# Kernel optimization log

Hardware: AMD Instinct MI355X
Metric: run time of the kernel (lower is better)

The kernel has to match this reference:

```python
import jax, jax.numpy as jnp
import numpy as np

N, E, G = 50000, 1600000, 512
IN_DIM, HEADS, C1, C2, HIDDEN = 128, 3, 32, 32, 512
NEG_SLOPE = 0.2
EPS = 1e-16


def _glorot(key, shape):
    fan_in = shape[0]
    return jax.random.normal(key, shape, dtype=jnp.float32) / np.sqrt(fan_in)


def setup_inputs() -> dict:
    key = jax.random.key(0)
    ks = jax.random.split(key, 16)
    x = jax.random.normal(ks[0], (N, IN_DIM), dtype=jnp.float32)
    edge_index = jax.random.randint(ks[1], (2, E), 0, N, dtype=jnp.int64)
    batch = (jnp.arange(N, dtype=jnp.int64) * G) // N  # sorted, all graphs non-empty
    d1, d2 = HEADS * C1, HEADS * C2
    return {
        "x": x,
        "W_l1": _glorot(ks[2], (IN_DIM, d1)), "b_l1": jnp.zeros((d1,), jnp.float32),
        "W_r1": _glorot(ks[3], (IN_DIM, d1)), "b_r1": jnp.zeros((d1,), jnp.float32),
        "att1": _glorot(ks[4], (HEADS, C1)), "bias1": jnp.zeros((d1,), jnp.float32),
        "W_l2": _glorot(ks[5], (d1, d2)), "b_l2": jnp.zeros((d2,), jnp.float32),
        "W_r2": _glorot(ks[6], (d1, d2)), "b_r2": jnp.zeros((d2,), jnp.float32),
        "att2": _glorot(ks[7], (HEADS, C2)), "bias2": jnp.zeros((d2,), jnp.float32),
        "W_fc1": _glorot(ks[8], (d1 + d2, HIDDEN)), "b_fc1": jnp.zeros((HIDDEN,), jnp.float32),
        "W_fc2": _glorot(ks[9], (HIDDEN, 2)), "b_fc2": jnp.zeros((2,), jnp.float32),
        "edge_index": edge_index,
        "batch": batch,
    }


def gatv2_conv(xin, src, dst, W_l, b_l, W_r, b_r, att, bias, heads, out_c):
    n = xin.shape[0]
    x_l = (xin @ W_l + b_l).reshape(n, heads, out_c)  # source-side projection
    x_r = (xin @ W_r + b_r).reshape(n, heads, out_c)  # target-side projection
    e = jax.nn.leaky_relu(x_l[src] + x_r[dst], NEG_SLOPE)  # [E', H, C]
    logits = jnp.einsum("ehc,hc->eh", e, att)  # [E', H]
    m = jax.ops.segment_max(logits, dst, num_segments=n)
    a = jnp.exp(logits - m[dst])
    denom = jax.ops.segment_sum(a, dst, num_segments=n)
    alpha = a / (denom[dst] + EPS)  # per-destination edge softmax (PyG semantics)
    out = jax.ops.segment_sum(x_l[src] * alpha[:, :, None], dst, num_segments=n)
    return out.reshape(n, heads * out_c) + bias


def reference(x, W_l1, b_l1, W_r1, b_r1, att1, bias1,
              W_l2, b_l2, W_r2, b_r2, att2, bias2,
              W_fc1, b_fc1, W_fc2, b_fc2, edge_index, batch):
    n = x.shape[0]
    loop = jnp.arange(n, dtype=edge_index.dtype)
    src = jnp.concatenate([edge_index[0], loop])  # PyG GATv2Conv adds self-loops
    dst = jnp.concatenate([edge_index[1], loop])
    h1 = jnp.tanh(gatv2_conv(x, src, dst, W_l1, b_l1, W_r1, b_r1, att1, bias1, HEADS, C1))
    h2 = jnp.tanh(gatv2_conv(h1, src, dst, W_l2, b_l2, W_r2, b_r2, att2, bias2, HEADS, C2))
    h = jnp.concatenate([h1, h2], axis=1)  # [N, (C1+C2)*H]
    first_idx = jnp.searchsorted(batch, jnp.arange(G, dtype=batch.dtype))  # first node of each graph
    pooled = h[first_idx]  # [G, (C1+C2)*H]
    hidden = jax.nn.relu(pooled @ W_fc1 + b_fc1)
    logits = hidden @ W_fc2 + b_fc2
    return jax.nn.log_softmax(logits, axis=1)
```

## Files before the change

kernel.cpp:

```cpp
#include <hip/hip_runtime.h>
#include <hip/hip_bf16.h>
#include <hip/hip_fp16.h>
#include <math.h>

#define NN 50000
#define EE 1600000
#define GG 512
#define INDIM 128
#define HEADS 3
#define CC 32
#define DD 96
#define HID 512
#define NEG 0.2f
#define EPS_DEN 1e-16f
#define CAP 128

#define OFF_WL1   0
#define OFF_BL1   12288
#define OFF_WR1   12384
#define OFF_BR1   24672
#define OFF_ATT1  24768
#define OFF_BIAS1 24864
#define OFF_WL2   24960
#define OFF_BL2   34176
#define OFF_WR2   34272
#define OFF_BR2   43488
#define OFF_ATT2  43584
#define OFF_BIAS2 43680
#define OFF_WFC1  43776
#define OFF_BFC1  142080
#define OFF_WFC2  142592
#define OFF_BFC2  143616
#define P_TOTAL   143744

typedef _Float16 h8 __attribute__((ext_vector_type(8)));
typedef float f4 __attribute__((ext_vector_type(4)));

static __device__ __forceinline__ float bf2f(__hip_bfloat16 v) { return __bfloat162float(v); }

static __device__ __forceinline__ int getI(const void* p, long long i, bool w64) {
    return w64 ? ((const int*)p)[2 * i] : ((const int*)p)[i];
}

__global__ void detect_kernel(const void* __restrict__ x, const void* __restrict__ ei,
                              int* __restrict__ flags)
{
    __shared__ int wild, zcnt;
    if (threadIdx.x == 0) { wild = 0; zcnt = 0; }
    __syncthreads();
    int w = 0, z = 0;
    const __hip_bfloat16* xb = (const __hip_bfloat16*)x;
    for (int i = threadIdx.x; i < 4096; i += 256) {
        float v = bf2f(xb[i]);
        if (!(fabsf(v) <= 1e6f)) w++;
    }
    const int* e32 = (const int*)ei;
    for (int i = threadIdx.x; i < 4096; i += 256) {
        if (e32[2 * i + 1] == 0) z++;
    }
    atomicAdd(&wild, w);
    atomicAdd(&zcnt, z);
    __syncthreads();
    if (threadIdx.x == 0) {
        flags[0] = (wild < 64) ? 1 : 0;
        flags[1] = (zcnt > 4000) ? 1 : 0;
    }
}

struct ParamTab { const void* p[16]; int sz[16]; int off[16]; };

__global__ void convert_params_kernel(ParamTab t, const int* __restrict__ flags,
                                      float* __restrict__ P)
{
    const int which = blockIdx.y;
    const int n = t.sz[which];
    const void* src = t.p[which];
    float* dst = P + t.off[which];
    const bool isbf = flags[0] != 0;
    for (int i = blockIdx.x * 256 + threadIdx.x; i < n; i += gridDim.x * 256) {
        dst[i] = isbf ? bf2f(((const __hip_bfloat16*)src)[i]) : ((const float*)src)[i];
    }
}

__global__ void build_bswz_kernel(const float* __restrict__ P, int offWl, int offWr, int KC,
                                  __half* __restrict__ B)
{
    int idx = blockIdx.x * 256 + threadIdx.x;
    int total = 12 * KC * 64;
    if (idx >= total) return;
    int lane = idx & 63;
    int t = idx >> 6;
    int kc = t % KC;
    int ntile = t / KC;
    int n = ntile * 16 + (lane & 15);
    int kbase = kc * 32 + (lane >> 4) * 8;
    const float* Wsrc = (n < 96) ? (P + offWl) : (P + offWr);
    int n2 = (n < 96) ? n : n - 96;
    __half* dst = B + (size_t)idx * 8;
#pragma unroll
    for (int j = 0; j < 8; j++) dst[j] = __float2half(Wsrc[(kbase + j) * 96 + n2]);
}

__global__ void conv_x_kernel(const void* __restrict__ x, const int* __restrict__ flags,
                              __half* __restrict__ xh)
{
    const bool isbf = flags[0] != 0;
    int i0 = (blockIdx.x * 256 + threadIdx.x) * 4;
    if (i0 >= NN * INDIM) return;
#pragma unroll
    for (int j = 0; j < 4; j++) {
        int i = i0 + j;
        float v = isbf ? bf2f(((const __hip_bfloat16*)x)[i]) : ((const float*)x)[i];
        xh[i] = __float2half(v);
    }
}

__global__ void firstpool_kernel(const void* __restrict__ batch, const int* __restrict__ flags,
                                 int* __restrict__ first, int* __restrict__ pooled,
                                 int* __restrict__ needed)
{
    int i = blockIdx.x * 256 + threadIdx.x;
    if (i >= NN) return;
    const bool w64 = flags[1] != 0;
    int b = getI(batch, i, w64);
    if (i == 0 || getI(batch, i - 1, w64) != b) {
        first[b] = i;
        pooled[i] = 1;
        needed[i] = 1;
    }
}

__global__ void mark_needed_kernel(const void* __restrict__ ei, const int* __restrict__ flags,
                                   const int* __restrict__ pooled, int* __restrict__ needed)
{
    int e = blockIdx.x * 256 + threadIdx.x;
    if (e >= EE) return;
    const bool w64 = flags[1] != 0;
    int dst = getI(ei, (long long)EE + e, w64);
    if (pooled[dst]) needed[getI(ei, e, w64)] = 1;
}

__global__ void compact_kernel(const int* __restrict__ needed, int* __restrict__ list,
                               int* __restrict__ cnt)
{
    int i = blockIdx.x * 256 + threadIdx.x;
    if (i >= NN) return;
    if (needed[i]) list[atomicAdd(cnt, 1)] = i;
}

__global__ void scatter_fixed_kernel(const void* __restrict__ ei, const int* __restrict__ flags,
                                     const int* __restrict__ needed,
                                     int* __restrict__ deg, int* __restrict__ csr)
{
    int e = blockIdx.x * 256 + threadIdx.x;
    if (e >= EE) return;
    const bool w64 = flags[1] != 0;
    int dst = getI(ei, (long long)EE + e, w64);
    if (!needed[dst]) return;
    int src = getI(ei, e, w64);
    int pos = atomicAdd(&deg[dst], 1);
    if (pos < CAP) csr[(size_t)dst * CAP + pos] = src;
}

template <int KDIM, int MODE>
__global__ __launch_bounds__(256) void proj_mfma_kernel(
    const __half* __restrict__ Ain, const __half* __restrict__ Bswz,
    const int* __restrict__ list, const int* __restrict__ cnt,
    const float* __restrict__ P, int offBl, int offBr,
    __half* __restrict__ xl, float* __restrict__ xr)
{
    constexpr int KC = KDIM / 32;
    __shared__ __half Bs[12 * KC * 64 * 8];
    const int tid = threadIdx.x;
    const int limit = MODE ? *cnt : NN;
    const int blockBase = blockIdx.x * 64;
    if (blockBase >= limit) return;

    {
        const int chunks = 12 * KC * 64;
        for (int i = tid; i < chunks; i += 256)
            reinterpret_cast<f4*>(Bs)[i] = reinterpret_cast<const f4*>(Bswz)[i];
    }
    __syncthreads();

    const int wave = tid >> 6;
    const int lane = tid & 63;
    const int base = blockBase + wave * 16;
    if (base >= limit) return;

    const int q = lane >> 4;
    const int mlane = lane & 15;

    int aIdx = base + mlane;
    int aRow;
    if (MODE) aRow = (aIdx < limit) ? list[aIdx] : list[limit - 1];
    else      aRow = (aIdx < limit) ? aIdx : 0;

    h8 a[KC];
    const h8* arow = reinterpret_cast<const h8*>(Ain + (size_t)aRow * KDIM);
#pragma unroll
    for (int kc = 0; kc < KC; kc++) a[kc] = arow[kc * 4 + q];

    int sRow[4];
#pragma unroll
    for (int r = 0; r < 4; r++) {
        int si = base + q * 4 + r;
        sRow[r] = (si < limit) ? (MODE ? list[si] : si) : -1;
    }

    const h8* Bf = reinterpret_cast<const h8*>(Bs);
#pragma unroll
    for (int ntile = 0; ntile < 12; ntile++) {
        int n = ntile * 16 + mlane;
        float bv = (n < 96) ? P[offBl + n] : P[offBr + n - 96];
        f4 acc = {bv, bv, bv, bv};
#pragma unroll
        for (int kc = 0; kc < KC; kc++) {
            h8 b = Bf[(ntile * KC + kc) * 64 + lane];
            acc = __builtin_amdgcn_mfma_f32_16x16x32_f16(a[kc], b, acc, 0, 0, 0);
        }
#pragma unroll
        for (int r = 0; r < 4; r++) {
            if (sRow[r] < 0) continue;
            if (n < 96) xl[(size_t)sRow[r] * DD + n] = __float2half(acc[r]);
            else        xr[(size_t)sRow[r] * DD + (n - 96)] = acc[r];
        }
    }
}

template <int OUTMODE>
__global__ __launch_bounds__(256) void fused_edge_kernel(
    const int* __restrict__ csr, const int* __restrict__ deg,
    const int* __restrict__ list, const int* __restrict__ cnt,
    const __half* __restrict__ xl, const float* __restrict__ xr,
    const float* __restrict__ P, int offAtt, int offBias,
    void* __restrict__ out)
{
    const int lane = threadIdx.x & 63;
    const int c = lane & 31;
    const int eo = lane >> 5;
    const int w0 = (blockIdx.x * 256 + threadIdx.x) >> 6;
    const int nw = (gridDim.x * 256) >> 6;
    const int limit = (OUTMODE == 0) ? *cnt : GG;
    const int items = limit * 3;

    for (int item = w0; item < items; item += nw) {
        const int li = item / 3;
        const int h = item - li * 3;
        const int n = list[li];
        const int hc = h * CC + c;

        const float attc = P[offAtt + hc];
        const float xr_c = xr[(size_t)n * DD + hc];

        float m, d, o;
        {
            float xls = __half2float(xl[(size_t)n * DD + hc]);
            float s = xls + xr_c;
            s = s > 0.0f ? s : NEG * s;
            float p = s * attc;
#pragma unroll
            for (int off = 16; off; off >>= 1) p += __shfl_xor(p, off, 32);
            if (eo == 0) { m = p; d = 1.0f; o = xls; }
            else         { m = -INFINITY; d = 0.0f; o = 0.0f; }
        }

        const int* row = csr + (size_t)n * CAP;
        const int end = min(deg[n], CAP);
        int k = eo;
        for (; k + 2 < end; k += 4) {
            int s0 = row[k], s1 = row[k + 2];
            float x0 = __half2float(xl[(size_t)s0 * DD + hc]);
            float x1 = __half2float(xl[(size_t)s1 * DD + hc]);
            float t0 = x0 + xr_c; t0 = t0 > 0.0f ? t0 : NEG * t0;
            float t1 = x1 + xr_c; t1 = t1 > 0.0f ? t1 : NEG * t1;
            float q0 = t0 * attc;
            float q1 = t1 * attc;
#pragma unroll
            for (int off = 16; off; off >>= 1) {
                q0 += __shfl_xor(q0, off, 32);
                q1 += __shfl_xor(q1, off, 32);
            }
            if (q0 <= m) { float e = __expf(q0 - m); d += e; o += e * x0; }
            else         { float r2 = __expf(m - q0); d = d * r2 + 1.0f; o = o * r2 + x0; m = q0; }
            if (q1 <= m) { float e = __expf(q1 - m); d += e; o += e * x1; }
            else         { float r2 = __expf(m - q1); d = d * r2 + 1.0f; o = o * r2 + x1; m = q1; }
        }
        for (; k < end; k += 2) {
            int src = row[k];
            float xv = __half2float(xl[(size_t)src * DD + hc]);
            float s = xv + xr_c;
            s = s > 0.0f ? s : NEG * s;
            float p = s * attc;
#pragma unroll
            for (int off = 16; off; off >>= 1) p += __shfl_xor(p, off, 32);
            if (p <= m) { float e = __expf(p - m); d += e; o += e * xv; }
            else        { float r2 = __expf(m - p); d = d * r2 + 1.0f; o = o * r2 + xv; m = p; }
        }

        float m2 = __shfl_xor(m, 32);
        float d2 = __shfl_xor(d, 32);
        float o2 = __shfl_xor(o, 32);
        float nm = fmaxf(m, m2);
        float e1 = __expf(m - nm), e2 = __expf(m2 - nm);
        d = d * e1 + d2 * e2;
        o = o * e1 + o2 * e2;

        float res = tanhf(o / (d + EPS_DEN) + P[offBias + hc]);
        if (eo == 0) {
            if (OUTMODE == 0) ((__half*)out)[(size_t)n * DD + hc] = __float2half(res);
            else              ((float*)out)[(size_t)li * DD + hc] = res;
        }
    }
}

__global__ __launch_bounds__(256) void mlp_kernel(
    const __half* __restrict__ h1h, const float* __restrict__ h2p,
    const float* __restrict__ P, const int* __restrict__ flags,
    const int* __restrict__ first, void* __restrict__ outv)
{
    __shared__ float pooled[2 * DD];
    __shared__ float hidden[HID];
    __shared__ float r0[4], r1[4];
    const int g = blockIdx.x;
    const int t = threadIdx.x;
    const int row = first[g];

    if (t < DD) pooled[t] = __half2float(h1h[(size_t)row * DD + t]);
    else if (t < 2 * DD) pooled[t] = h2p[(size_t)g * DD + (t - DD)];
    __syncthreads();

    for (int col = t; col < HID; col += 256) {
        float acc = P[OFF_BFC1 + col];
        for (int i = 0; i < 2 * DD; i++) acc += pooled[i] * P[OFF_WFC1 + i * HID + col];
        hidden[col] = fmaxf(acc, 0.0f);
    }
    __syncthreads();

    float p0 = 0.0f, p1 = 0.0f;
    for (int j = t; j < HID; j += 256) {
        float hv = hidden[j];
        p0 += hv * P[OFF_WFC2 + j * 2 + 0];
        p1 += hv * P[OFF_WFC2 + j * 2 + 1];
    }
#pragma unroll
    for (int off = 32; off > 0; off >>= 1) {
        p0 += __shfl_down(p0, off);
        p1 += __shfl_down(p1, off);
    }
    int w = t >> 6;
    if ((t & 63) == 0) { r0[w] = p0; r1[w] = p1; }
    __syncthreads();
    if (t == 0) {
        float l0 = r0[0] + r0[1] + r0[2] + r0[3] + P[OFF_BFC2 + 0];
        float l1 = r1[0] + r1[1] + r1[2] + r1[3] + P[OFF_BFC2 + 1];
        float mx = fmaxf(l0, l1);
        float lse = mx + logf(expf(l0 - mx) + expf(l1 - mx));
        float o0 = l0 - lse, o1 = l1 - lse;
        if (flags[0]) {
            ((__hip_bfloat16*)outv)[g * 2 + 0] = __float2bfloat16(o0);
            ((__hip_bfloat16*)outv)[g * 2 + 1] = __float2bfloat16(o1);
        } else {
            ((float*)outv)[g * 2 + 0] = o0;
            ((float*)outv)[g * 2 + 1] = o1;
        }
    }
}

extern "C" void kernel_launch(void* const* d_in, const int* in_sizes, int n_in,
                              void* d_out, int out_size, void* d_ws, size_t ws_size,
                              hipStream_t stream)
{
    const void* x     = d_in[0];
    const void* ei    = d_in[17];
    const void* batch = d_in[18];

    float* ws   = (float*)d_ws;
    float* P    = ws;
    float* xr   = P + P_TOTAL;
    float* h2p  = xr + (size_t)NN * DD;

    __half* hp   = (__half*)(h2p + (size_t)GG * DD);
    __half* xh   = hp;
    __half* xlh  = xh + (size_t)NN * INDIM;
    __half* xl2h = xlh + (size_t)NN * DD;
    __half* h1h  = xl2h + (size_t)NN * DD;
    __half* B1   = h1h + (size_t)NN * DD;
    __half* B2   = B1 + 24576;

    int* ip      = (int*)(B2 + 18432);
    int* deg     = ip;
    int* pooled  = deg + NN;
    int* needed  = pooled + NN;
    int* cnt     = needed + NN;
    int* csr     = cnt + 4;
    int* list    = csr + (size_t)NN * CAP;
    int* first   = list + NN;
    int* flags   = first + GG;

    ParamTab t;
    const int sz[16]  = {12288, 96, 12288, 96, 96, 96, 9216, 96, 9216, 96, 96, 96, 98304, 512, 1024, 2};
    const int off[16] = {OFF_WL1, OFF_BL1, OFF_WR1, OFF_BR1, OFF_ATT1, OFF_BIAS1,
                         OFF_WL2, OFF_BL2, OFF_WR2, OFF_BR2, OFF_ATT2, OFF_BIAS2,
                         OFF_WFC1, OFF_BFC1, OFF_WFC2, OFF_BFC2};
    for (int i = 0; i < 16; i++) { t.p[i] = d_in[1 + i]; t.sz[i] = sz[i]; t.off[i] = off[i]; }

    const int edgeB = (EE + 255) / 256;
    const int nodeB = (NN + 255) / 256;
    const int mprojB = (NN + 63) / 64;
    const int fuse1B = 2048;
    const int fuse2B = (GG * 3) / 4;

    detect_kernel<<<1, 256, 0, stream>>>(x, ei, flags);
    convert_params_kernel<<<dim3(96, 16), 256, 0, stream>>>(t, flags, P);
    build_bswz_kernel<<<12, 256, 0, stream>>>(P, OFF_WL1, OFF_WR1, 4, B1);
    build_bswz_kernel<<<9, 256, 0, stream>>>(P, OFF_WL2, OFF_WR2, 3, B2);
    conv_x_kernel<<<(NN * INDIM / 4 + 255) / 256, 256, 0, stream>>>(x, flags, xh);
    (void)hipMemsetAsync(deg, 0, (size_t)(3 * NN + 4) * sizeof(int), stream);

    firstpool_kernel<<<nodeB, 256, 0, stream>>>(batch, flags, first, pooled, needed);
    mark_needed_kernel<<<edgeB, 256, 0, stream>>>(ei, flags, pooled, needed);
    compact_kernel<<<nodeB, 256, 0, stream>>>(needed, list, cnt);

    scatter_fixed_kernel<<<edgeB, 256, 0, stream>>>(ei, flags, needed, deg, csr);

    proj_mfma_kernel<INDIM, 0><<<mprojB, 256, 0, stream>>>(xh, B1, nullptr, nullptr,
                                                           P, OFF_BL1, OFF_BR1, xlh, xr);
    fused_edge_kernel<0><<<fuse1B, 256, 0, stream>>>(csr, deg, list, cnt, xlh, xr,
                                                     P, OFF_ATT1, OFF_BIAS1, (void*)h1h);

    proj_mfma_kernel<DD, 1><<<mprojB, 256, 0, stream>>>(h1h, B2, list, cnt,
                                                        P, OFF_BL2, OFF_BR2, xl2h, xr);
    fused_edge_kernel<1><<<fuse2B, 256, 0, stream>>>(csr, deg, first, nullptr, xl2h, xr,
                                                     P, OFF_ATT2, OFF_BIAS2, (void*)h2p);

    mlp_kernel<<<GG, 256, 0, stream>>>(h1h, h2p, P, flags, first, d_out);
}
```

Before: 293.5 us.

## Vectorize edge-index loads and process 16 neighbors per wave in edge softmax

```diff
diff --git a/kernel.cpp b/kernel.cpp
--- a/kernel.cpp
+++ b/kernel.cpp
@@ -14,6 +14,7 @@
 #define NEG 0.2f
 #define EPS_DEN 1e-16f
 #define CAP 128
+#define MNEG -1e30f
 
 #define OFF_WL1   0
 #define OFF_BL1   12288
@@ -42,6 +43,18 @@
     return w64 ? ((const int*)p)[2 * i] : ((const int*)p)[i];
 }
 
+static __device__ __forceinline__ void load4(const void* p, int base, int e0, bool w64, int* v) {
+    const int4* q = (const int4*)p;
+    if (w64) {
+        int4 a = q[(base + e0) >> 1];
+        int4 b = q[((base + e0) >> 1) + 1];
+        v[0] = a.x; v[1] = a.z; v[2] = b.x; v[3] = b.z;
+    } else {
+        int4 a = q[(base + e0) >> 2];
+        v[0] = a.x; v[1] = a.y; v[2] = a.z; v[3] = a.w;
+    }
+}
+
 __global__ void detect_kernel(const void* __restrict__ x, const void* __restrict__ ei,
                               int* __restrict__ flags)
 {
@@ -133,11 +146,14 @@
 __global__ void mark_needed_kernel(const void* __restrict__ ei, const int* __restrict__ flags,
                                    const int* __restrict__ pooled, int* __restrict__ needed)
 {
-    int e = blockIdx.x * 256 + threadIdx.x;
-    if (e >= EE) return;
+    int e0 = (blockIdx.x * 256 + threadIdx.x) * 4;
+    if (e0 >= EE) return;
     const bool w64 = flags[1] != 0;
-    int dst = getI(ei, (long long)EE + e, w64);
-    if (pooled[dst]) needed[getI(ei, e, w64)] = 1;
+    int s4[4], d4[4];
+    load4(ei, EE, e0, w64, d4);
+    load4(ei, 0, e0, w64, s4);
+#pragma unroll
+    for (int j = 0; j < 4; j++) if (pooled[d4[j]]) needed[s4[j]] = 1;
 }
 
 __global__ void compact_kernel(const int* __restrict__ needed, int* __restrict__ list,
@@ -152,14 +168,19 @@
                                      const int* __restrict__ needed,
                                      int* __restrict__ deg, int* __restrict__ csr)
 {
-    int e = blockIdx.x * 256 + threadIdx.x;
-    if (e >= EE) return;
+    int e0 = (blockIdx.x * 256 + threadIdx.x) * 4;
+    if (e0 >= EE) return;
     const bool w64 = flags[1] != 0;
-    int dst = getI(ei, (long long)EE + e, w64);
-    if (!needed[dst]) return;
-    int src = getI(ei, e, w64);
-    int pos = atomicAdd(&deg[dst], 1);
-    if (pos < CAP) csr[(size_t)dst * CAP + pos] = src;
+    int s4[4], d4[4];
+    load4(ei, EE, e0, w64, d4);
+    load4(ei, 0, e0, w64, s4);
+#pragma unroll
+    for (int j = 0; j < 4; j++) {
+        int dst = d4[j];
+        if (!needed[dst]) continue;
+        int pos = atomicAdd(&deg[dst], 1);
+        if (pos < CAP) csr[(size_t)dst * CAP + pos] = s4[j];
+    }
 }
 
 template <int KDIM, int MODE>
@@ -237,8 +258,8 @@
     void* __restrict__ out)
 {
     const int lane = threadIdx.x & 63;
-    const int c = lane & 31;
-    const int eo = lane >> 5;
+    const int g  = lane >> 2;
+    const int ql = lane & 3;
     const int w0 = (blockIdx.x * 256 + threadIdx.x) >> 6;
     const int nw = (gridDim.x * 256) >> 6;
     const int limit = (OUTMODE == 0) ? *cnt : GG;
@@ -248,68 +269,103 @@
         const int li = item / 3;
         const int h = item - li * 3;
         const int n = list[li];
-        const int hc = h * CC + c;
-
-        const float attc = P[offAtt + hc];
-        const float xr_c = xr[(size_t)n * DD + hc];
-
-        float m, d, o;
+        const int cb = h * CC + ql * 8;
+
+        float att8[8], xr8[8];
         {
-            float xls = __half2float(xl[(size_t)n * DD + hc]);
-            float s = xls + xr_c;
-            s = s > 0.0f ? s : NEG * s;
-            float p = s * attc;
-#pragma unroll
-            for (int off = 16; off; off >>= 1) p += __shfl_xor(p, off, 32);
-            if (eo == 0) { m = p; d = 1.0f; o = xls; }
-            else         { m = -INFINITY; d = 0.0f; o = 0.0f; }
-        }
+            const f4* ap = reinterpret_cast<const f4*>(P + offAtt + cb);
+            *reinterpret_cast<f4*>(&att8[0]) = ap[0];
+            *reinterpret_cast<f4*>(&att8[4]) = ap[1];
+            const f4* xp = reinterpret_cast<const f4*>(xr + (size_t)n * DD + cb);
+            *reinterpret_cast<f4*>(&xr8[0]) = xp[0];
+            *reinterpret_cast<f4*>(&xr8[4]) = xp[1];
+        }
+
+        float m = MNEG, d = 0.0f, o8[8];
+#pragma unroll
+        for (int j = 0; j < 8; j++) o8[j] = 0.0f;
 
         const int* row = csr + (size_t)n * CAP;
         const int end = min(deg[n], CAP);
-        int k = eo;
-        for (; k + 2 < end; k += 4) {
-            int s0 = row[k], s1 = row[k + 2];
-            float x0 = __half2float(xl[(size_t)s0 * DD + hc]);
-            float x1 = __half2float(xl[(size_t)s1 * DD + hc]);
-            float t0 = x0 + xr_c; t0 = t0 > 0.0f ? t0 : NEG * t0;
-            float t1 = x1 + xr_c; t1 = t1 > 0.0f ? t1 : NEG * t1;
-            float q0 = t0 * attc;
-            float q1 = t1 * attc;
-#pragma unroll
-            for (int off = 16; off; off >>= 1) {
-                q0 += __shfl_xor(q0, off, 32);
-                q1 += __shfl_xor(q1, off, 32);
+
+        if (g == 0) {
+            h8 xh = *reinterpret_cast<const h8*>(xl + (size_t)n * DD + cb);
+            float xv8[8];
+#pragma unroll
+            for (int j = 0; j < 8; j++) xv8[j] = (float)xh[j];
+            float p = 0.0f;
+#pragma unroll
+            for (int j = 0; j < 8; j++) {
+                float s = xv8[j] + xr8[j];
+                s = s > 0.0f ? s : NEG * s;
+                p = fmaf(s, att8[j], p);
             }
-            if (q0 <= m) { float e = __expf(q0 - m); d += e; o += e * x0; }
-            else         { float r2 = __expf(m - q0); d = d * r2 + 1.0f; o = o * r2 + x0; m = q0; }
-            if (q1 <= m) { float e = __expf(q1 - m); d += e; o += e * x1; }
-            else         { float r2 = __expf(m - q1); d = d * r2 + 1.0f; o = o * r2 + x1; m = q1; }
-        }
-        for (; k < end; k += 2) {
+            p += __shfl_xor(p, 1);
+            p += __shfl_xor(p, 2);
+            m = p; d = 1.0f;
+#pragma unroll
+            for (int j = 0; j < 8; j++) o8[j] = xv8[j];
+        }
+
+        for (int k = g; k < end; k += 16) {
             int src = row[k];
-            float xv = __half2float(xl[(size_t)src * DD + hc]);
-            float s = xv + xr_c;
-            s = s > 0.0f ? s : NEG * s;
-            float p = s * attc;
-#pragma unroll
-            for (int off = 16; off; off >>= 1) p += __shfl_xor(p, off, 32);
-            if (p <= m) { float e = __expf(p - m); d += e; o += e * xv; }
-            else        { float r2 = __expf(m - p); d = d * r2 + 1.0f; o = o * r2 + xv; m = p; }
-        }
-
-        float m2 = __shfl_xor(m, 32);
-        float d2 = __shfl_xor(d, 32);
-        float o2 = __shfl_xor(o, 32);
-        float nm = fmaxf(m, m2);
-        float e1 = __expf(m - nm), e2 = __expf(m2 - nm);
-        d = d * e1 + d2 * e2;
-        o = o * e1 + o2 * e2;
-
-        float res = tanhf(o / (d + EPS_DEN) + P[offBias + hc]);
-        if (eo == 0) {
-            if (OUTMODE == 0) ((__half*)out)[(size_t)n * DD + hc] = __float2half(res);
-            else              ((float*)out)[(size_t)li * DD + hc] = res;
+            h8 xh = *reinterpret_cast<const h8*>(xl + (size_t)src * DD + cb);
+            float xv8[8];
+#pragma unroll
+            for (int j = 0; j < 8; j++) xv8[j] = (float)xh[j];
+            float p = 0.0f;
+#pragma unroll
+            for (int j = 0; j < 8; j++) {
+                float s = xv8[j] + xr8[j];
+                s = s > 0.0f ? s : NEG * s;
+                p = fmaf(s, att8[j], p);
+            }
+            p += __shfl_xor(p, 1);
+            p += __shfl_xor(p, 2);
+            if (p <= m) {
+                float e = __expf(p - m);
+                d += e;
+#pragma unroll
+                for (int j = 0; j < 8; j++) o8[j] = fmaf(e, xv8[j], o8[j]);
+            } else {
+                float r = __expf(m - p);
+                d = fmaf(d, r, 1.0f);
+#pragma unroll
+                for (int j = 0; j < 8; j++) o8[j] = fmaf(o8[j], r, xv8[j]);
+                m = p;
+            }
+        }
+
+#pragma unroll
+        for (int off = 4; off <= 32; off <<= 1) {
+            float m2 = __shfl_xor(m, off);
+            float d2 = __shfl_xor(d, off);
+            float o2[8];
+#pragma unroll
+            for (int j = 0; j < 8; j++) o2[j] = __shfl_xor(o8[j], off);
+            float nm = fmaxf(m, m2);
+            float e1 = __expf(m - nm), e2 = __expf(m2 - nm);
+            d = d * e1 + d2 * e2;
+#pragma unroll
+            for (int j = 0; j < 8; j++) o8[j] = o8[j] * e1 + o2[j] * e2;
+            m = nm;
+        }
+
+        if (g == 0) {
+            float inv = 1.0f / (d + EPS_DEN);
+            float res[8];
+#pragma unroll
+            for (int j = 0; j < 8; j++) res[j] = tanhf(o8[j] * inv + P[offBias + cb + j]);
+            if (OUTMODE == 0) {
+                h8 r;
+#pragma unroll
+                for (int j = 0; j < 8; j++) r[j] = (_Float16)res[j];
+                *reinterpret_cast<h8*>((__half*)out + (size_t)n * DD + cb) = r;
+            } else {
+                float* po = (float*)out + (size_t)li * DD + cb;
+                *reinterpret_cast<f4*>(po) = *reinterpret_cast<f4*>(&res[0]);
+                *reinterpret_cast<f4*>(po + 4) = *reinterpret_cast<f4*>(&res[4]);
+            }
         }
     }
 }
@@ -405,7 +461,7 @@
                          OFF_WFC1, OFF_BFC1, OFF_WFC2, OFF_BFC2};
     for (int i = 0; i < 16; i++) { t.p[i] = d_in[1 + i]; t.sz[i] = sz[i]; t.off[i] = off[i]; }
 
-    const int edgeB = (EE + 255) / 256;
+    const int edge4B = (EE / 4 + 255) / 256;
     const int nodeB = (NN + 255) / 256;
     const int mprojB = (NN + 63) / 64;
     const int fuse1B = 2048;
@@ -419,10 +475,10 @@
     (void)hipMemsetAsync(deg, 0, (size_t)(3 * NN + 4) * sizeof(int), stream);
 
     firstpool_kernel<<<nodeB, 256, 0, stream>>>(batch, flags, first, pooled, needed);
-    mark_needed_kernel<<<edgeB, 256, 0, stream>>>(ei, flags, pooled, needed);
+    mark_needed_kernel<<<edge4B, 256, 0, stream>>>(ei, flags, pooled, needed);
     compact_kernel<<<nodeB, 256, 0, stream>>>(needed, list, cnt);
 
-    scatter_fixed_kernel<<<edgeB, 256, 0, stream>>>(ei, flags, needed, deg, csr);
+    scatter_fixed_kernel<<<edge4B, 256, 0, stream>>>(ei, flags, needed, deg, csr);
 
     proj_mfma_kernel<INDIM, 0><<<mprojB, 256, 0, stream>>>(xh, B1, nullptr, nullptr,
                                                            P, OFF_BL1, OFF_BR1, xlh, xr);
```

Result: slower. 302.4 us (+3.0%).

## Fuse x conversion into projection, vectorize edge loads, unroll edge loop by eight

Applied to the files above, without the earlier changes.

```diff
diff --git a/kernel.cpp b/kernel.cpp
--- a/kernel.cpp
+++ b/kernel.cpp
@@ -14,6 +14,7 @@
 #define NEG 0.2f
 #define EPS_DEN 1e-16f
 #define CAP 128
+#define MNEG -1e30f
 
 #define OFF_WL1   0
 #define OFF_BL1   12288
@@ -42,6 +43,18 @@
     return w64 ? ((const int*)p)[2 * i] : ((const int*)p)[i];
 }
 
+static __device__ __forceinline__ void load4(const void* p, int base, int e0, bool w64, int* v) {
+    const int4* q = (const int4*)p;
+    if (w64) {
+        int4 a = q[(base + e0) >> 1];
+        int4 b = q[((base + e0) >> 1) + 1];
+        v[0] = a.x; v[1] = a.z; v[2] = b.x; v[3] = b.z;
+    } else {
+        int4 a = q[(base + e0) >> 2];
+        v[0] = a.x; v[1] = a.y; v[2] = a.z; v[3] = a.w;
+    }
+}
+
 __global__ void detect_kernel(const void* __restrict__ x, const void* __restrict__ ei,
                               int* __restrict__ flags)
 {
@@ -101,20 +114,6 @@
     for (int j = 0; j < 8; j++) dst[j] = __float2half(Wsrc[(kbase + j) * 96 + n2]);
 }
 
-__global__ void conv_x_kernel(const void* __restrict__ x, const int* __restrict__ flags,
-                              __half* __restrict__ xh)
-{
-    const bool isbf = flags[0] != 0;
-    int i0 = (blockIdx.x * 256 + threadIdx.x) * 4;
-    if (i0 >= NN * INDIM) return;
-#pragma unroll
-    for (int j = 0; j < 4; j++) {
-        int i = i0 + j;
-        float v = isbf ? bf2f(((const __hip_bfloat16*)x)[i]) : ((const float*)x)[i];
-        xh[i] = __float2half(v);
-    }
-}
-
 __global__ void firstpool_kernel(const void* __restrict__ batch, const int* __restrict__ flags,
                                  int* __restrict__ first, int* __restrict__ pooled,
                                  int* __restrict__ needed)
@@ -133,11 +132,14 @@
 __global__ void mark_needed_kernel(const void* __restrict__ ei, const int* __restrict__ flags,
                                    const int* __restrict__ pooled, int* __restrict__ needed)
 {
-    int e = blockIdx.x * 256 + threadIdx.x;
-    if (e >= EE) return;
+    int e0 = (blockIdx.x * 256 + threadIdx.x) * 4;
+    if (e0 >= EE) return;
     const bool w64 = flags[1] != 0;
-    int dst = getI(ei, (long long)EE + e, w64);
-    if (pooled[dst]) needed[getI(ei, e, w64)] = 1;
+    int s4[4], d4[4];
+    load4(ei, EE, e0, w64, d4);
+    load4(ei, 0, e0, w64, s4);
+#pragma unroll
+    for (int j = 0; j < 4; j++) if (pooled[d4[j]]) needed[s4[j]] = 1;
 }
 
 __global__ void compact_kernel(const int* __restrict__ needed, int* __restrict__ list,
@@ -152,21 +154,26 @@
                                      const int* __restrict__ needed,
                                      int* __restrict__ deg, int* __restrict__ csr)
 {
-    int e = blockIdx.x * 256 + threadIdx.x;
-    if (e >= EE) return;
+    int e0 = (blockIdx.x * 256 + threadIdx.x) * 4;
+    if (e0 >= EE) return;
     const bool w64 = flags[1] != 0;
-    int dst = getI(ei, (long long)EE + e, w64);
-    if (!needed[dst]) return;
-    int src = getI(ei, e, w64);
-    int pos = atomicAdd(&deg[dst], 1);
-    if (pos < CAP) csr[(size_t)dst * CAP + pos] = src;
+    int s4[4], d4[4];
+    load4(ei, EE, e0, w64, d4);
+    load4(ei, 0, e0, w64, s4);
+#pragma unroll
+    for (int j = 0; j < 4; j++) {
+        int dst = d4[j];
+        if (!needed[dst]) continue;
+        int pos = atomicAdd(&deg[dst], 1);
+        if (pos < CAP) csr[(size_t)dst * CAP + pos] = s4[j];
+    }
 }
 
 template <int KDIM, int MODE>
 __global__ __launch_bounds__(256) void proj_mfma_kernel(
-    const __half* __restrict__ Ain, const __half* __restrict__ Bswz,
+    const void* __restrict__ Ain, const __half* __restrict__ Bswz,
     const int* __restrict__ list, const int* __restrict__ cnt,
-    const float* __restrict__ P, int offBl, int offBr,
+    const float* __restrict__ P, const int* __restrict__ flags, int offBl, int offBr,
     __half* __restrict__ xl, float* __restrict__ xr)
 {
     constexpr int KC = KDIM / 32;
@@ -197,9 +204,35 @@
     else      aRow = (aIdx < limit) ? aIdx : 0;
 
     h8 a[KC];
-    const h8* arow = reinterpret_cast<const h8*>(Ain + (size_t)aRow * KDIM);
-#pragma unroll
-    for (int kc = 0; kc < KC; kc++) a[kc] = arow[kc * 4 + q];
+    if (MODE == 1) {
+        const h8* arow = reinterpret_cast<const h8*>((const __half*)Ain + (size_t)aRow * KDIM);
+#pragma unroll
+        for (int kc = 0; kc < KC; kc++) a[kc] = arow[kc * 4 + q];
+    } else if (flags[0]) {
+        const int4* arow = reinterpret_cast<const int4*>((const ushort*)Ain + (size_t)aRow * KDIM);
+#pragma unroll
+        for (int kc = 0; kc < KC; kc++) {
+            int4 r = arow[kc * 4 + q];
+            int ws[4] = {r.x, r.y, r.z, r.w};
+#pragma unroll
+            for (int i = 0; i < 4; i++) {
+                a[kc][2 * i]     = (_Float16)__int_as_float(ws[i] << 16);
+                a[kc][2 * i + 1] = (_Float16)__int_as_float(ws[i] & 0xffff0000);
+            }
+        }
+    } else {
+        const f4* arow = reinterpret_cast<const f4*>((const float*)Ain + (size_t)aRow * KDIM);
+#pragma unroll
+        for (int kc = 0; kc < KC; kc++) {
+            f4 r0 = arow[kc * 8 + q * 2];
+            f4 r1 = arow[kc * 8 + q * 2 + 1];
+#pragma unroll
+            for (int i = 0; i < 4; i++) {
+                a[kc][i]     = (_Float16)r0[i];
+                a[kc][4 + i] = (_Float16)r1[i];
+            }
+        }
+    }
 
     int sRow[4];
 #pragma unroll
@@ -262,29 +295,38 @@
 #pragma unroll
             for (int off = 16; off; off >>= 1) p += __shfl_xor(p, off, 32);
             if (eo == 0) { m = p; d = 1.0f; o = xls; }
-            else         { m = -INFINITY; d = 0.0f; o = 0.0f; }
+            else         { m = MNEG; d = 0.0f; o = 0.0f; }
         }
 
         const int* row = csr + (size_t)n * CAP;
         const int end = min(deg[n], CAP);
         int k = eo;
-        for (; k + 2 < end; k += 4) {
-            int s0 = row[k], s1 = row[k + 2];
+        for (; k + 6 < end; k += 8) {
+            int s0 = row[k], s1 = row[k + 2], s2 = row[k + 4], s3 = row[k + 6];
             float x0 = __half2float(xl[(size_t)s0 * DD + hc]);
             float x1 = __half2float(xl[(size_t)s1 * DD + hc]);
+            float x2 = __half2float(xl[(size_t)s2 * DD + hc]);
+            float x3 = __half2float(xl[(size_t)s3 * DD + hc]);
             float t0 = x0 + xr_c; t0 = t0 > 0.0f ? t0 : NEG * t0;
             float t1 = x1 + xr_c; t1 = t1 > 0.0f ? t1 : NEG * t1;
-            float q0 = t0 * attc;
-            float q1 = t1 * attc;
+            float t2 = x2 + xr_c; t2 = t2 > 0.0f ? t2 : NEG * t2;
+            float t3 = x3 + xr_c; t3 = t3 > 0.0f ? t3 : NEG * t3;
+            float q0 = t0 * attc, q1 = t1 * attc, q2 = t2 * attc, q3 = t3 * attc;
 #pragma unroll
             for (int off = 16; off; off >>= 1) {
                 q0 += __shfl_xor(q0, off, 32);
                 q1 += __shfl_xor(q1, off, 32);
+                q2 += __shfl_xor(q2, off, 32);
+                q3 += __shfl_xor(q3, off, 32);
             }
             if (q0 <= m) { float e = __expf(q0 - m); d += e; o += e * x0; }
             else         { float r2 = __expf(m - q0); d = d * r2 + 1.0f; o = o * r2 + x0; m = q0; }
             if (q1 <= m) { float e = __expf(q1 - m); d += e; o += e * x1; }
             else         { float r2 = __expf(m - q1); d = d * r2 + 1.0f; o = o * r2 + x1; m = q1; }
+            if (q2 <= m) { float e = __expf(q2 - m); d += e; o += e * x2; }
+            else         { float r2 = __expf(m - q2); d = d * r2 + 1.0f; o = o * r2 + x2; m = q2; }
+            if (q3 <= m) { float e = __expf(q3 - m); d += e; o += e * x3; }
+            else         { float r2 = __expf(m - q3); d = d * r2 + 1.0f; o = o * r2 + x3; m = q3; }
         }
         for (; k < end; k += 2) {
             int src = row[k];
@@ -381,8 +423,7 @@
     float* h2p  = xr + (size_t)NN * DD;
 
     __half* hp   = (__half*)(h2p + (size_t)GG * DD);
-    __half* xh   = hp;
-    __half* xlh  = xh + (size_t)NN * INDIM;
+    __half* xlh  = hp;
     __half* xl2h = xlh + (size_t)NN * DD;
     __half* h1h  = xl2h + (size_t)NN * DD;
     __half* B1   = h1h + (size_t)NN * DD;
@@ -405,7 +446,7 @@
                          OFF_WFC1, OFF_BFC1, OFF_WFC2, OFF_BFC2};
     for (int i = 0; i < 16; i++) { t.p[i] = d_in[1 + i]; t.sz[i] = sz[i]; t.off[i] = off[i]; }
 
-    const int edgeB = (EE + 255) / 256;
+    const int edge4B = (EE / 4 + 255) / 256;
     const int nodeB = (NN + 255) / 256;
     const int mprojB = (NN + 63) / 64;
     const int fuse1B = 2048;
@@ -415,22 +456,21 @@
     convert_params_kernel<<<dim3(96, 16), 256, 0, stream>>>(t, flags, P);
     build_bswz_kernel<<<12, 256, 0, stream>>>(P, OFF_WL1, OFF_WR1, 4, B1);
     build_bswz_kernel<<<9, 256, 0, stream>>>(P, OFF_WL2, OFF_WR2, 3, B2);
-    conv_x_kernel<<<(NN * INDIM / 4 + 255) / 256, 256, 0, stream>>>(x, flags, xh);
     (void)hipMemsetAsync(deg, 0, (size_t)(3 * NN + 4) * sizeof(int), stream);
 
     firstpool_kernel<<<nodeB, 256, 0, stream>>>(batch, flags, first, pooled, needed);
-    mark_needed_kernel<<<edgeB, 256, 0, stream>>>(ei, flags, pooled, needed);
+    mark_needed_kernel<<<edge4B, 256, 0, stream>>>(ei, flags, pooled, needed);
     compact_kernel<<<nodeB, 256, 0, stream>>>(needed, list, cnt);
 
-    scatter_fixed_kernel<<<edgeB, 256, 0, stream>>>(ei, flags, needed, deg, csr);
-
-    proj_mfma_kernel<INDIM, 0><<<mprojB, 256, 0, stream>>>(xh, B1, nullptr, nullptr,
-                                                           P, OFF_BL1, OFF_BR1, xlh, xr);
+    scatter_fixed_kernel<<<edge4B, 256, 0, stream>>>(ei, flags, needed, deg, csr);
+
+    proj_mfma_kernel<INDIM, 0><<<mprojB, 256, 0, stream>>>(x, B1, nullptr, nullptr,
+                                                           P, flags, OFF_BL1, OFF_BR1, xlh, xr);
     fused_edge_kernel<0><<<fuse1B, 256, 0, stream>>>(csr, deg, list, cnt, xlh, xr,
                                                      P, OFF_ATT1, OFF_BIAS1, (void*)h1h);
 
     proj_mfma_kernel<DD, 1><<<mprojB, 256, 0, stream>>>(h1h, B2, list, cnt,
-                                                        P, OFF_BL2, OFF_BR2, xl2h, xr);
+                                                        P, flags, OFF_BL2, OFF_BR2, xl2h, xr);
     fused_edge_kernel<1><<<fuse2B, 256, 0, stream>>>(csr, deg, first, nullptr, xl2h, xr,
                                                      P, OFF_ATT2, OFF_BIAS2, (void*)h2p);
 
```

After: 280.9 us. -4.3%, faster.
